# Kernel optimization log

Hardware: AMD Instinct MI355X
Metric: run time of the kernel (lower is better)

The kernel has to match this reference:

```python
import jax, jax.numpy as jnp
import numpy as np

M = 65536  # total flattened feature length (sum of ragged segment lengths n_k)
K = 4096   # number of segments (sub-networks)
B = 256    # batch size


def setup_inputs() -> dict:
    key = jax.random.key(0)
    k1, k2, k3 = jax.random.split(key, 3)
    x = jax.random.normal(k1, (B, 1, M), dtype=jnp.float32)
    w = jax.random.normal(k2, (M,), dtype=jnp.float32)
    # contiguous ragged segments: sorted segment ids in [0, K)
    seg_ids = jnp.sort(jax.random.randint(k3, (M,), 0, K, dtype=jnp.int32))
    return {"x": x, "w": w, "seg_ids": seg_ids, "num_segments": K}


def reference(x, w, seg_ids, num_segments):
    # GINN input layer: for each batch row, slice the flat input into K ragged
    # contiguous segments, dot each segment with the matching slice of the flat
    # weight vector, concatenate the K scalars, apply tanh.
    # Equivalent fused form: u2[b,k] = sum_{i in seg k} w[i]*x[b,0,i]; out = tanh(u2)
    xs = x[:, 0, :]                      # [B, M]
    prod = xs * w                        # [B, M] elementwise
    seg_sum = jax.vmap(
        lambda p: jax.ops.segment_sum(p, seg_ids, num_segments=num_segments)
    )(prod)                              # [B, K]
    return jnp.tanh(seg_sum)
```

## Files before the change

### kernel.cpp

```cpp
#include <hip/hip_runtime.h>


#define TPB 64
#define CH  1280
#define VPT (CH / TPB / 4)

__global__ void build_seg_ptr_scatter(const int* __restrict__ seg_ids,
                                      int* __restrict__ seg_ptr,
                                      int M, int K) {
    int m = blockIdx.x * blockDim.x + threadIdx.x;
    if (m >= M) return;
    int a  = seg_ids[m];
    int nb = (m + 1 < M) ? seg_ids[m + 1] : K;
    if (m == 0) {
        for (int k = 0; k <= a; ++k) seg_ptr[k] = 0;
    }
    for (int k = a + 1; k <= nb; ++k) seg_ptr[k] = m + 1;
}

__global__ __launch_bounds__(TPB) void seg_reduce_tanh(
        const float* __restrict__ x,
        const float* __restrict__ w,
        const int* __restrict__ seg_ptr,
        float* __restrict__ out,
        int M, int K) {
    __shared__ float prod[CH];

    const int t  = threadIdx.x;
    const int k0 = blockIdx.x * TPB;
    const int b  = blockIdx.y;
    const float* __restrict__ xb = x + (size_t)b * (size_t)M;

    const int s    = seg_ptr[k0];
    const int e    = seg_ptr[k0 + TPB];
    const int base = s & ~3;
    const int a_t  = seg_ptr[k0 + t];
    const int b_t  = seg_ptr[k0 + t + 1];

    float sum = 0.0f;
    for (int c = base; c < e; c += CH) {
        const float4* __restrict__ x4 = reinterpret_cast<const float4*>(xb + c);
        const float4* __restrict__ w4 = reinterpret_cast<const float4*>(w + c);
        float4* __restrict__ p4 = reinterpret_cast<float4*>(prod);
        #pragma unroll
        for (int j = 0; j < VPT; ++j) {
            int idx = t + j * TPB;
            int mm  = c + idx * 4;
            float4 v = make_float4(0.f, 0.f, 0.f, 0.f);
            if (mm < e) {
                float4 xv = x4[idx];
                float4 wv = w4[idx];
                v.x = xv.x * wv.x; v.y = xv.y * wv.y;
                v.z = xv.z * wv.z; v.w = xv.w * wv.w;
            }
            p4[idx] = v;
        }
        __syncthreads();
        int lo = max(a_t, c);
        int hi = min(b_t, c + CH);
        for (int m = lo; m < hi; ++m) sum += prod[m - c];
        __syncthreads();
    }
    out[(size_t)b * (size_t)K + k0 + t] = tanhf(sum);
}

extern "C" void kernel_launch(void* const* d_in, const int* in_sizes, int n_in,
                              void* d_out, int out_size, void* d_ws, size_t ws_size,
                              hipStream_t stream) {
    const float* x       = (const float*)d_in[0];
    const float* w       = (const float*)d_in[1];
    const int*   seg_ids = (const int*)d_in[2];
    float* out = (float*)d_out;

    const int M = in_sizes[1];
    const int B = in_sizes[0] / M;
    const int K = out_size / B;

    int* seg_ptr = (int*)d_ws;

    build_seg_ptr_scatter<<<(M + 255) / 256, 256, 0, stream>>>(seg_ids, seg_ptr, M, K);

    dim3 grid(K / TPB, B);
    seg_reduce_tanh<<<grid, TPB, 0, stream>>>(x, w, seg_ptr, out, M, K);
}
```

Before: 25.77 us.

## Fuse segment-pointer build into reduce kernel via per-block binary search

Drops the separate scatter kernel that built segment offsets. Each block now finds its own segment boundaries by binary searching the sorted seg_ids and stores them in shared memory. The per-thread accumulation loop now reads shared memory as float4 and masks the edges. This saves a kernel launch and a dependency on a global workspace, but every block in the B×K/64 grid repeats about 16 dependent global loads per thread for the search.

```diff
diff --git a/kernel.cpp b/kernel.cpp
--- a/kernel.cpp
+++ b/kernel.cpp
@@ -5,37 +5,47 @@
 #define CH  1280
 #define VPT (CH / TPB / 4)
 
-__global__ void build_seg_ptr_scatter(const int* __restrict__ seg_ids,
-                                      int* __restrict__ seg_ptr,
-                                      int M, int K) {
-    int m = blockIdx.x * blockDim.x + threadIdx.x;
-    if (m >= M) return;
-    int a  = seg_ids[m];
-    int nb = (m + 1 < M) ? seg_ids[m + 1] : K;
-    if (m == 0) {
-        for (int k = 0; k <= a; ++k) seg_ptr[k] = 0;
-    }
-    for (int k = a + 1; k <= nb; ++k) seg_ptr[k] = m + 1;
-}
-
-__global__ __launch_bounds__(TPB) void seg_reduce_tanh(
+__global__ __launch_bounds__(TPB) void fused_seg_reduce_tanh(
         const float* __restrict__ x,
         const float* __restrict__ w,
-        const int* __restrict__ seg_ptr,
+        const int* __restrict__ seg_ids,
         float* __restrict__ out,
         int M, int K) {
-    __shared__ float prod[CH];
+    __shared__ __align__(16) float prod[CH];
+    __shared__ int sp[TPB + 1];
 
     const int t  = threadIdx.x;
     const int k0 = blockIdx.x * TPB;
     const int b  = blockIdx.y;
     const float* __restrict__ xb = x + (size_t)b * (size_t)M;
 
-    const int s    = seg_ptr[k0];
-    const int e    = seg_ptr[k0 + TPB];
+    {
+        int tgt = k0 + t;
+        int lo = 0, hi = M;
+        while (lo < hi) {
+            int mid = (lo + hi) >> 1;
+            bool lt = seg_ids[mid] < tgt;
+            lo = lt ? mid + 1 : lo;
+            hi = lt ? hi : mid;
+        }
+        sp[t] = lo;
+        int tgt2 = k0 + TPB;
+        int lo2 = 0, hi2 = M;
+        while (lo2 < hi2) {
+            int mid = (lo2 + hi2) >> 1;
+            bool lt = seg_ids[mid] < tgt2;
+            lo2 = lt ? mid + 1 : lo2;
+            hi2 = lt ? hi2 : mid;
+        }
+        sp[TPB] = lo2;
+    }
+    __syncthreads();
+
+    const int s    = sp[0];
+    const int e    = sp[TPB];
     const int base = s & ~3;
-    const int a_t  = seg_ptr[k0 + t];
-    const int b_t  = seg_ptr[k0 + t + 1];
+    const int a_t  = sp[t];
+    const int b_t  = sp[t + 1];
 
     float sum = 0.0f;
     for (int c = base; c < e; c += CH) {
@@ -56,9 +66,16 @@
             p4[idx] = v;
         }
         __syncthreads();
-        int lo = max(a_t, c);
-        int hi = min(b_t, c + CH);
-        for (int m = lo; m < hi; ++m) sum += prod[m - c];
+        int lo = max(a_t, c) - c;
+        int hi = min(b_t, c + CH) - c;
+        int r0 = lo & ~3;
+        for (int r = r0; r < hi; r += 4) {
+            float4 v = *reinterpret_cast<const float4*>(&prod[r]);
+            sum += (r + 0 >= lo && r + 0 < hi) ? v.x : 0.0f;
+            sum += (r + 1 >= lo && r + 1 < hi) ? v.y : 0.0f;
+            sum += (r + 2 >= lo && r + 2 < hi) ? v.z : 0.0f;
+            sum += (r + 3 >= lo && r + 3 < hi) ? v.w : 0.0f;
+        }
         __syncthreads();
     }
     out[(size_t)b * (size_t)K + k0 + t] = tanhf(sum);
@@ -76,10 +93,6 @@
     const int B = in_sizes[0] / M;
     const int K = out_size / B;
 
-    int* seg_ptr = (int*)d_ws;
-
-    build_seg_ptr_scatter<<<(M + 255) / 256, 256, 0, stream>>>(seg_ids, seg_ptr, M, K);
-
     dim3 grid(K / TPB, B);
-    seg_reduce_tanh<<<grid, TPB, 0, stream>>>(x, w, seg_ptr, out, M, K);
+    fused_seg_reduce_tanh<<<grid, TPB, 0, stream>>>(x, w, seg_ids, out, M, K);
 }
```

Measured after the change: 32.35 us. +25.5%, slower.

## Replace per-segment serial sums with wavefront prefix scan and two batch rows per block

Applied to the files above, without the earlier changes.

Each thread now loads a contiguous run of 20 x*w products into registers, forms a local running sum, and combines runs with a wave-wide shuffle scan into an inclusive prefix array in shared memory. Each segment's sum then comes from the difference of two prefix entries instead of a serial loop over its elements. This removes the divergent, length-dependent per-thread accumulation. Each block also handles two batch rows so the weight loads are shared, which halves the grid and uses more registers. Prefix differencing changes the floating-point summation order and can add rounding error on long chunks.

```diff
diff --git a/kernel.cpp b/kernel.cpp
--- a/kernel.cpp
+++ b/kernel.cpp
@@ -1,9 +1,12 @@
 #include <hip/hip_runtime.h>
 
 
-#define TPB 64
-#define CH  1280
-#define VPT (CH / TPB / 4)
+#define SEGB 64
+#define NB   2
+#define TPB  64
+#define LPT  20
+#define CH   (64 * LPT)
+#define F4L  (LPT / 4)
 
 __global__ void build_seg_ptr_scatter(const int* __restrict__ seg_ids,
                                       int* __restrict__ seg_ptr,
@@ -18,50 +21,85 @@
     for (int k = a + 1; k <= nb; ++k) seg_ptr[k] = m + 1;
 }
 
-__global__ __launch_bounds__(TPB) void seg_reduce_tanh(
+__global__ __launch_bounds__(TPB) void seg_prefix_tanh(
         const float* __restrict__ x,
         const float* __restrict__ w,
-        const int* __restrict__ seg_ptr,
+        const int* __restrict__ sp,
         float* __restrict__ out,
         int M, int K) {
-    __shared__ float prod[CH];
+    __shared__ __align__(16) float I[NB][CH];
 
-    const int t  = threadIdx.x;
-    const int k0 = blockIdx.x * TPB;
-    const int b  = blockIdx.y;
-    const float* __restrict__ xb = x + (size_t)b * (size_t)M;
+    const int ln = threadIdx.x;
+    const int k0 = blockIdx.x * SEGB;
+    const int b0 = blockIdx.y * NB;
+    const int M4 = M >> 2;
 
-    const int s    = seg_ptr[k0];
-    const int e    = seg_ptr[k0 + TPB];
+    const int s   = sp[k0];
+    const int e   = sp[k0 + SEGB];
+    const int a_t = sp[k0 + ln];
+    const int b_t = sp[k0 + ln + 1];
     const int base = s & ~3;
-    const int a_t  = seg_ptr[k0 + t];
-    const int b_t  = seg_ptr[k0 + t + 1];
 
-    float sum = 0.0f;
+    const float4* __restrict__ w4 = reinterpret_cast<const float4*>(w);
+    const float4* __restrict__ x4a = reinterpret_cast<const float4*>(x + (size_t)(b0 + 0) * M);
+    const float4* __restrict__ x4b = reinterpret_cast<const float4*>(x + (size_t)(b0 + 1) * M);
+
+    float sum0 = 0.0f, sum1 = 0.0f;
+
     for (int c = base; c < e; c += CH) {
-        const float4* __restrict__ x4 = reinterpret_cast<const float4*>(xb + c);
-        const float4* __restrict__ w4 = reinterpret_cast<const float4*>(w + c);
-        float4* __restrict__ p4 = reinterpret_cast<float4*>(prod);
+        const int f40 = (c >> 2) + ln * F4L;
+        float4 wq[F4L], xqa[F4L], xqb[F4L];
         #pragma unroll
-        for (int j = 0; j < VPT; ++j) {
-            int idx = t + j * TPB;
-            int mm  = c + idx * 4;
-            float4 v = make_float4(0.f, 0.f, 0.f, 0.f);
-            if (mm < e) {
-                float4 xv = x4[idx];
-                float4 wv = w4[idx];
-                v.x = xv.x * wv.x; v.y = xv.y * wv.y;
-                v.z = xv.z * wv.z; v.w = xv.w * wv.w;
+        for (int j = 0; j < F4L; ++j) {
+            int f4 = min(f40 + j, M4 - 1);
+            wq[j]  = w4[f4];
+            xqa[j] = x4a[f4];
+            xqb[j] = x4b[f4];
+        }
+        #pragma unroll
+        for (int bb = 0; bb < NB; ++bb) {
+            float L[LPT];
+            float run = 0.0f;
+            #pragma unroll
+            for (int j = 0; j < F4L; ++j) {
+                float4 xv = (bb == 0) ? xqa[j] : xqb[j];
+                run = fmaf(xv.x, wq[j].x, run); L[j*4+0] = run;
+                run = fmaf(xv.y, wq[j].y, run); L[j*4+1] = run;
+                run = fmaf(xv.z, wq[j].z, run); L[j*4+2] = run;
+                run = fmaf(xv.w, wq[j].w, run); L[j*4+3] = run;
             }
-            p4[idx] = v;
+            float S = run;
+            #pragma unroll
+            for (int d = 1; d < 64; d <<= 1) {
+                float u = __shfl_up(S, d);
+                if (ln >= d) S += u;
+            }
+            const float E = S - run;
+            float4* Ip4 = reinterpret_cast<float4*>(&I[bb][ln * LPT]);
+            #pragma unroll
+            for (int j = 0; j < F4L; ++j) {
+                Ip4[j] = make_float4(L[j*4+0] + E, L[j*4+1] + E,
+                                     L[j*4+2] + E, L[j*4+3] + E);
+            }
         }
         __syncthreads();
-        int lo = max(a_t, c);
-        int hi = min(b_t, c + CH);
-        for (int m = lo; m < hi; ++m) sum += prod[m - c];
+        {
+            int lo = max(a_t, c) - c;
+            int hi = min(b_t, c + CH) - c;
+            if (hi > lo) {
+                float ph0 = I[0][hi - 1];
+                float pl0 = (lo > 0) ? I[0][lo - 1] : 0.0f;
+                float ph1 = I[1][hi - 1];
+                float pl1 = (lo > 0) ? I[1][lo - 1] : 0.0f;
+                sum0 += ph0 - pl0;
+                sum1 += ph1 - pl1;
+            }
+        }
         __syncthreads();
     }
-    out[(size_t)b * (size_t)K + k0 + t] = tanhf(sum);
+
+    out[(size_t)(b0 + 0) * K + k0 + ln] = tanhf(sum0);
+    out[(size_t)(b0 + 1) * K + k0 + ln] = tanhf(sum1);
 }
 
 extern "C" void kernel_launch(void* const* d_in, const int* in_sizes, int n_in,
@@ -80,6 +118,6 @@
 
     build_seg_ptr_scatter<<<(M + 255) / 256, 256, 0, stream>>>(seg_ids, seg_ptr, M, K);
 
-    dim3 grid(K / TPB, B);
-    seg_reduce_tanh<<<grid, TPB, 0, stream>>>(x, w, seg_ptr, out, M, K);
+    dim3 grid(K / SEGB, B / NB);
+    seg_prefix_tanh<<<grid, TPB, 0, stream>>>(x, w, seg_ptr, out, M, K);
 }
```

Measured after the change: 29.06 us. +12.7%, slower.
